# Kernel tuning notes

Measured on AMD Instinct MI355X. Metric: run time of the kernel, lower is better.

## Reference

```python
import jax, jax.numpy as jnp
import numpy as np

B, T, C = 2048, 200, 128
PAD = jnp.float32(-4294967295.0)  # -(2**32) + 1, as in SoftmaxWeightedSum padding


def setup_inputs() -> dict:
    key = jax.random.key(0)
    k1, k2, k3, k4 = jax.random.split(key, 4)
    user_query = jax.random.normal(k1, (B, 1, C), dtype=jnp.float32)
    keys = jax.random.normal(k2, (B, T, C), dtype=jnp.float32)
    keys_length = jax.random.randint(k3, (B, 1), 0, T, dtype=jnp.int32)
    W = jax.random.normal(k4, (C, C), dtype=jnp.float32) * (1.0 / np.sqrt(C))
    b = jnp.zeros((C,), dtype=jnp.float32)
    return {"user_query": user_query, "keys": keys, "keys_length": keys_length, "W": W, "b": b}


def reference(user_query, keys, keys_length, W, b):
    # Dense with tanh activation: [B,1,C] -> [B,1,C]
    query = jnp.tanh(jnp.einsum('bqc,cd->bqd', user_query, W) + b)
    # DotAttention with scale: [B,1,T]
    scale = jnp.asarray(1.0 / np.sqrt(C), dtype=keys.dtype)
    align = jnp.einsum('bqc,btc->bqt', query, keys) * scale
    # sequence mask [B,1,T] from keys_length [B,1]
    key_masks = jnp.arange(T, dtype=keys_length.dtype)[None, None, :] < keys_length[:, :, None]
    align = jnp.where(key_masks, align, PAD)
    align = jax.nn.softmax(align, axis=-1)
    # weighted sum over history: [B,1,C]
    output = jnp.einsum('bqt,btc->bqc', align, keys)
    # residual: broadcasts [B,1,C] + [B,T,C] -> [B,T,C] (faithful to `output += keys`)
    output = output + keys
    # mean pool over sequence, keepdims -> [B,1,C]
    return jnp.mean(output, axis=1, keepdims=True)
```

## Files before the change

### kernel.cpp

```cpp
#include <hip/hip_runtime.h>
#include <math.h>

#define BB 2048
#define TT 200
#define CC 128
#define PADV (-4294967295.0f)
#define SCALE 0.08838834764831845f
#define INV_T (1.0f / 200.0f)

__global__ __launch_bounds__(256) void q_gemv_kernel(
    const float* __restrict__ uq,
    const float* __restrict__ W,
    const float* __restrict__ bias,
    float*       __restrict__ qws)
{
    const int tid = threadIdx.x;
    const int d   = tid & 127;
    const int wh  = tid >> 7;
    const int b   = blockIdx.x * 2 + wh;

    __shared__ float s_uq[2 * CC];
    s_uq[tid] = uq[blockIdx.x * 2 * CC + tid];
    __syncthreads();

    float acc = bias[d];
    const float* uqr = &s_uq[wh * CC];
    #pragma unroll 16
    for (int c = 0; c < CC; ++c)
        acc = fmaf(uqr[c], W[c * CC + d], acc);
    qws[(size_t)b * CC + d] = tanhf(acc);
}

__global__ __launch_bounds__(256, 6) void attn_stream_kernel(
    const float* __restrict__ keys,
    const int*   __restrict__ klen,
    const float* __restrict__ qws,
    float*       __restrict__ out)
{
    const int b    = blockIdx.x;
    const int tid  = threadIdx.x;
    const int lane = tid & 63;
    const int wid  = tid >> 6;
    const int cl   = lane & 31;
    const int h    = lane >> 5;
    const int g    = wid * 2 + h;
    const int c4   = cl * 4;

    __shared__ float  s_m[8];
    __shared__ float  s_l[8];
    __shared__ float4 s_acc[8 * 32];
    __shared__ float4 s_ksum[8 * 32];

    const float* kb  = keys + (size_t)b * TT * CC;
    const int    len = klen[b];
    const float4 q   = *(const float4*)(qws + (size_t)b * CC + c4);

    float  m = -INFINITY, l = 0.0f;
    float4 acc  = make_float4(0.f, 0.f, 0.f, 0.f);
    float4 ksum = make_float4(0.f, 0.f, 0.f, 0.f);

    auto upd = [&](float d, const float4& k, int r) {
        const float s  = (r < len) ? d * SCALE : PADV;
        const float mn = fmaxf(m, s);
        const float sc = __expf(m - mn);
        const float p  = __expf(s - mn);
        l = fmaf(l, sc, p);
        acc.x = fmaf(p, k.x, acc.x * sc);
        acc.y = fmaf(p, k.y, acc.y * sc);
        acc.z = fmaf(p, k.z, acc.z * sc);
        acc.w = fmaf(p, k.w, acc.w * sc);
        ksum.x += k.x; ksum.y += k.y; ksum.z += k.z; ksum.w += k.w;
        m = mn;
    };

    for (int outer = 0; outer < 5; ++outer) {
        const int r0 = g + 40 * outer;
        const float4 k0 = *(const float4*)(kb + (r0     ) * CC + c4);
        const float4 k1 = *(const float4*)(kb + (r0 +  8) * CC + c4);
        const float4 k2 = *(const float4*)(kb + (r0 + 16) * CC + c4);
        const float4 k3 = *(const float4*)(kb + (r0 + 24) * CC + c4);
        const float4 k4 = *(const float4*)(kb + (r0 + 32) * CC + c4);

        float d0 = q.x * k0.x + q.y * k0.y + q.z * k0.z + q.w * k0.w;
        float d1 = q.x * k1.x + q.y * k1.y + q.z * k1.z + q.w * k1.w;
        float d2 = q.x * k2.x + q.y * k2.y + q.z * k2.z + q.w * k2.w;
        float d3 = q.x * k3.x + q.y * k3.y + q.z * k3.z + q.w * k3.w;
        float d4 = q.x * k4.x + q.y * k4.y + q.z * k4.z + q.w * k4.w;

        #pragma unroll
        for (int off = 1; off < 32; off <<= 1) {
            d0 += __shfl_xor(d0, off, 64);
            d1 += __shfl_xor(d1, off, 64);
            d2 += __shfl_xor(d2, off, 64);
            d3 += __shfl_xor(d3, off, 64);
            d4 += __shfl_xor(d4, off, 64);
        }

        upd(d0, k0, r0);
        upd(d1, k1, r0 + 8);
        upd(d2, k2, r0 + 16);
        upd(d3, k3, r0 + 24);
        upd(d4, k4, r0 + 32);
    }

    s_acc [g * 32 + cl] = acc;
    s_ksum[g * 32 + cl] = ksum;
    if (cl == 0) { s_m[g] = m; s_l[g] = l; }
    __syncthreads();

    if (tid < 32) {
        float M = s_m[0];
        #pragma unroll
        for (int i = 1; i < 8; ++i) M = fmaxf(M, s_m[i]);

        float  L  = 0.0f;
        float4 A  = make_float4(0.f, 0.f, 0.f, 0.f);
        float4 KS = make_float4(0.f, 0.f, 0.f, 0.f);
        #pragma unroll
        for (int i = 0; i < 8; ++i) {
            const float al = __expf(s_m[i] - M);
            L = fmaf(s_l[i], al, L);
            const float4 a = s_acc[i * 32 + tid];
            A.x = fmaf(a.x, al, A.x);
            A.y = fmaf(a.y, al, A.y);
            A.z = fmaf(a.z, al, A.z);
            A.w = fmaf(a.w, al, A.w);
            const float4 ks = s_ksum[i * 32 + tid];
            KS.x += ks.x; KS.y += ks.y; KS.z += ks.z; KS.w += ks.w;
        }
        const float invL = 1.0f / L;
        float4 o;
        o.x = fmaf(A.x, invL, KS.x * INV_T);
        o.y = fmaf(A.y, invL, KS.y * INV_T);
        o.z = fmaf(A.z, invL, KS.z * INV_T);
        o.w = fmaf(A.w, invL, KS.w * INV_T);
        *(float4*)(out + (size_t)b * CC + 4 * tid) = o;
    }
}

extern "C" void kernel_launch(void* const* d_in, const int* in_sizes, int n_in,
                              void* d_out, int out_size, void* d_ws, size_t ws_size,
                              hipStream_t stream) {
    const float* uq   = (const float*)d_in[0];
    const float* keys = (const float*)d_in[1];
    const int*   klen = (const int*)d_in[2];
    const float* W    = (const float*)d_in[3];
    const float* bias = (const float*)d_in[4];
    float* out = (float*)d_out;
    float* qws = (float*)d_ws;

    q_gemv_kernel<<<BB / 2, 256, 0, stream>>>(uq, W, bias, qws);
    attn_stream_kernel<<<BB, 256, 0, stream>>>(keys, klen, qws, out);
}
```

Measured before the change: 300.6 us.

## Fuse query GEMV into attention kernel with register double-buffered key loads

Computes the tanh(Wq+b) query projection inside the attention kernel, with two thread halves each reducing 64 input channels in shared memory. This removes the second launch and the query round-trip through workspace. The key stream is now software-prefetched one tile of five rows ahead in registers. The online softmax is batched over five rows per step, so each step does one rescale instead of five. Each block now re-reads the 64KB W matrix, which should mostly hit in cache. Occupancy is lowered to 4 waves per SIMD to make room for the extra registers.

```diff
diff --git a/kernel.cpp b/kernel.cpp
--- a/kernel.cpp
+++ b/kernel.cpp
@@ -8,33 +8,12 @@
 #define SCALE 0.08838834764831845f
 #define INV_T (1.0f / 200.0f)
 
-__global__ __launch_bounds__(256) void q_gemv_kernel(
+__global__ __launch_bounds__(256, 4) void user_attn_fused(
     const float* __restrict__ uq,
+    const float* __restrict__ keys,
+    const int*   __restrict__ klen,
     const float* __restrict__ W,
     const float* __restrict__ bias,
-    float*       __restrict__ qws)
-{
-    const int tid = threadIdx.x;
-    const int d   = tid & 127;
-    const int wh  = tid >> 7;
-    const int b   = blockIdx.x * 2 + wh;
-
-    __shared__ float s_uq[2 * CC];
-    s_uq[tid] = uq[blockIdx.x * 2 * CC + tid];
-    __syncthreads();
-
-    float acc = bias[d];
-    const float* uqr = &s_uq[wh * CC];
-    #pragma unroll 16
-    for (int c = 0; c < CC; ++c)
-        acc = fmaf(uqr[c], W[c * CC + d], acc);
-    qws[(size_t)b * CC + d] = tanhf(acc);
-}
-
-__global__ __launch_bounds__(256, 6) void attn_stream_kernel(
-    const float* __restrict__ keys,
-    const int*   __restrict__ klen,
-    const float* __restrict__ qws,
     float*       __restrict__ out)
 {
     const int b    = blockIdx.x;
@@ -46,46 +25,53 @@
     const int g    = wid * 2 + h;
     const int c4   = cl * 4;
 
+    __shared__ float  s_uq[CC];
+    __shared__ float  s_part[2 * CC];
+    __shared__ float  s_q[CC];
     __shared__ float  s_m[8];
     __shared__ float  s_l[8];
     __shared__ float4 s_acc[8 * 32];
     __shared__ float4 s_ksum[8 * 32];
 
-    const float* kb  = keys + (size_t)b * TT * CC;
+    if (tid < CC) s_uq[tid] = uq[(size_t)b * CC + tid];
+    __syncthreads();
+    {
+        const int d    = tid & 127;
+        const int part = tid >> 7;
+        const int c0   = part * 64;
+        float a = 0.0f;
+        #pragma unroll 16
+        for (int c = 0; c < 64; ++c)
+            a = fmaf(s_uq[c0 + c], W[(c0 + c) * CC + d], a);
+        s_part[part * CC + d] = a;
+    }
+    __syncthreads();
+    if (tid < CC) s_q[tid] = tanhf(bias[tid] + s_part[tid] + s_part[CC + tid]);
+    __syncthreads();
+
     const int    len = klen[b];
-    const float4 q   = *(const float4*)(qws + (size_t)b * CC + c4);
+    const float4 q   = *(const float4*)&s_q[c4];
+    const float4* kp = (const float4*)(keys + (size_t)b * TT * CC) + g * 32 + cl;
 
     float  m = -INFINITY, l = 0.0f;
     float4 acc  = make_float4(0.f, 0.f, 0.f, 0.f);
     float4 ksum = make_float4(0.f, 0.f, 0.f, 0.f);
 
-    auto upd = [&](float d, const float4& k, int r) {
-        const float s  = (r < len) ? d * SCALE : PADV;
-        const float mn = fmaxf(m, s);
-        const float sc = __expf(m - mn);
-        const float p  = __expf(s - mn);
-        l = fmaf(l, sc, p);
-        acc.x = fmaf(p, k.x, acc.x * sc);
-        acc.y = fmaf(p, k.y, acc.y * sc);
-        acc.z = fmaf(p, k.z, acc.z * sc);
-        acc.w = fmaf(p, k.w, acc.w * sc);
-        ksum.x += k.x; ksum.y += k.y; ksum.z += k.z; ksum.w += k.w;
-        m = mn;
-    };
+    float4 c0_ = kp[0], c1_ = kp[256], c2_ = kp[512], c3_ = kp[768], c4_ = kp[1024];
 
-    for (int outer = 0; outer < 5; ++outer) {
-        const int r0 = g + 40 * outer;
-        const float4 k0 = *(const float4*)(kb + (r0     ) * CC + c4);
-        const float4 k1 = *(const float4*)(kb + (r0 +  8) * CC + c4);
-        const float4 k2 = *(const float4*)(kb + (r0 + 16) * CC + c4);
-        const float4 k3 = *(const float4*)(kb + (r0 + 24) * CC + c4);
-        const float4 k4 = *(const float4*)(kb + (r0 + 32) * CC + c4);
+    #pragma unroll
+    for (int j = 0; j < 5; ++j) {
+        float4 n0, n1, n2, n3, n4;
+        if (j < 4) {
+            const float4* np = kp + 1280 * (j + 1);
+            n0 = np[0]; n1 = np[256]; n2 = np[512]; n3 = np[768]; n4 = np[1024];
+        }
 
-        float d0 = q.x * k0.x + q.y * k0.y + q.z * k0.z + q.w * k0.w;
-        float d1 = q.x * k1.x + q.y * k1.y + q.z * k1.z + q.w * k1.w;
-        float d2 = q.x * k2.x + q.y * k2.y + q.z * k2.z + q.w * k2.w;
-        float d3 = q.x * k3.x + q.y * k3.y + q.z * k3.z + q.w * k3.w;
-        float d4 = q.x * k4.x + q.y * k4.y + q.z * k4.z + q.w * k4.w;
+        float d0 = q.x * c0_.x + q.y * c0_.y + q.z * c0_.z + q.w * c0_.w;
+        float d1 = q.x * c1_.x + q.y * c1_.y + q.z * c1_.z + q.w * c1_.w;
+        float d2 = q.x * c2_.x + q.y * c2_.y + q.z * c2_.z + q.w * c2_.w;
+        float d3 = q.x * c3_.x + q.y * c3_.y + q.z * c3_.z + q.w * c3_.w;
+        float d4 = q.x * c4_.x + q.y * c4_.y + q.z * c4_.z + q.w * c4_.w;
 
         #pragma unroll
         for (int off = 1; off < 32; off <<= 1) {
@@ -96,11 +82,33 @@
             d4 += __shfl_xor(d4, off, 64);
         }
 
-        upd(d0, k0, r0);
-        upd(d1, k1, r0 + 8);
-        upd(d2, k2, r0 + 16);
-        upd(d3, k3, r0 + 24);
-        upd(d4, k4, r0 + 32);
+        const int r0 = g + 40 * j;
+        const float s0 = (r0      < len) ? d0 * SCALE : PADV;
+        const float s1 = (r0 +  8 < len) ? d1 * SCALE : PADV;
+        const float s2 = (r0 + 16 < len) ? d2 * SCALE : PADV;
+        const float s3 = (r0 + 24 < len) ? d3 * SCALE : PADV;
+        const float s4 = (r0 + 32 < len) ? d4 * SCALE : PADV;
+
+        const float gm = fmaxf(fmaxf(fmaxf(s0, s1), fmaxf(s2, s3)), s4);
+        const float mn = fmaxf(m, gm);
+        const float sc = __expf(m - mn);
+        const float p0 = __expf(s0 - mn);
+        const float p1 = __expf(s1 - mn);
+        const float p2 = __expf(s2 - mn);
+        const float p3 = __expf(s3 - mn);
+        const float p4 = __expf(s4 - mn);
+        l = fmaf(l, sc, ((p0 + p1) + (p2 + p3)) + p4);
+        acc.x = fmaf(p0, c0_.x, fmaf(p1, c1_.x, fmaf(p2, c2_.x, fmaf(p3, c3_.x, fmaf(p4, c4_.x, acc.x * sc)))));
+        acc.y = fmaf(p0, c0_.y, fmaf(p1, c1_.y, fmaf(p2, c2_.y, fmaf(p3, c3_.y, fmaf(p4, c4_.y, acc.y * sc)))));
+        acc.z = fmaf(p0, c0_.z, fmaf(p1, c1_.z, fmaf(p2, c2_.z, fmaf(p3, c3_.z, fmaf(p4, c4_.z, acc.z * sc)))));
+        acc.w = fmaf(p0, c0_.w, fmaf(p1, c1_.w, fmaf(p2, c2_.w, fmaf(p3, c3_.w, fmaf(p4, c4_.w, acc.w * sc)))));
+        ksum.x += ((c0_.x + c1_.x) + (c2_.x + c3_.x)) + c4_.x;
+        ksum.y += ((c0_.y + c1_.y) + (c2_.y + c3_.y)) + c4_.y;
+        ksum.z += ((c0_.z + c1_.z) + (c2_.z + c3_.z)) + c4_.z;
+        ksum.w += ((c0_.w + c1_.w) + (c2_.w + c3_.w)) + c4_.w;
+        m = mn;
+
+        c0_ = n0; c1_ = n1; c2_ = n2; c3_ = n3; c4_ = n4;
     }
 
     s_acc [g * 32 + cl] = acc;
@@ -147,8 +155,6 @@
     const float* W    = (const float*)d_in[3];
     const float* bias = (const float*)d_in[4];
     float* out = (float*)d_out;
-    float* qws = (float*)d_ws;
 
-    q_gemv_kernel<<<BB / 2, 256, 0, stream>>>(uq, W, bias, qws);
-    attn_stream_kernel<<<BB, 256, 0, stream>>>(keys, klen, qws, out);
+    user_attn_fused<<<BB, 256, 0, stream>>>(uq, keys, klen, W, bias, out);
 }
```

Measured after the change: 299.8 us. About the same (-0.3%).
